# Kernel optimization log

Hardware: AMD Instinct MI355X
Metric: run time of the kernel (lower is better)

The kernel has to match this reference:

```python
import jax, jax.numpy as jnp
import numpy as np

LRELU_GAIN = 2.0 ** 0.5  # util.lrelu_gain (assumed sqrt(2))
EPS = 1e-8


def upsample2_bilinear_ac(x):
    # F.upsample_bilinear == bilinear with align_corners=True, scale 2
    B, C, H, W = x.shape
    def lerp_axis(t, n, axis):
        c = jnp.arange(2 * n, dtype=jnp.float32) * (n - 1) / (2 * n - 1)
        i0 = jnp.floor(c).astype(jnp.int32)
        i1 = jnp.minimum(i0 + 1, n - 1)
        f = c - i0.astype(jnp.float32)
        a = jnp.take(t, i0, axis=axis)
        b = jnp.take(t, i1, axis=axis)
        shape = [1] * t.ndim
        shape[axis] = 2 * n
        f = f.reshape(shape)
        return a * (1.0 - f) + b * f
    x = lerp_axis(x, H, 2)
    x = lerp_axis(x, W, 3)
    return x


def conv1x1(x, weight, bias, gain):
    # Conv2dNormalizedLR with kernel_size=1: he = gain/sqrt(in)
    cin = weight.shape[1]
    he = gain / float(cin) ** 0.5
    y = jnp.einsum('bihw,oi->bohw', x, weight[:, :, 0, 0] * he)
    return y + bias[None, :, None, None]


def mod_conv3x3(x, weight, style, gain):
    # weight: [Cin, Cout, 3, 3]; style: [B, Cin]
    cin, cout, k, _ = weight.shape
    he = gain / float(cin * k * k) ** 0.5
    wmod = style[:, :, None, None, None] * (weight * he)[None]  # [B,Cin,Cout,k,k]
    # demodulation: normalize over (in, kh, kw) per out channel
    d = jax.lax.rsqrt(jnp.sum(wmod * wmod, axis=(1, 3, 4), keepdims=True) + EPS)
    wmod = wmod * d
    # conv_transpose2d(stride=1, pad=1, k=3) == conv2d with transposed+flipped kernel, pad=1
    kern = jnp.flip(jnp.transpose(wmod, (0, 2, 1, 3, 4)), axis=(3, 4))  # [B,Cout,Cin,k,k]
    def one(xb, kb):
        return jax.lax.conv_general_dilated(
            xb[None], kb, (1, 1), ((1, 1), (1, 1)),
            dimension_numbers=('NCHW', 'OIHW', 'NCHW'))[0]
    y = jax.vmap(one)(x, kern)
    return y * gain


def noise_affine(noise, w_s, b_s, w_b, b_b):
    # Baff*: 1x1 conv from 1 channel, gain=1 -> he=1
    ys = noise * w_s[None, :, 0, None, 0, None][:, :, :, 0] if False else noise * w_s[:, 0, 0, 0][None, :, None, None] + b_s[None, :, None, None]
    yb = noise * w_b[:, 0, 0, 0][None, :, None, None] + b_b[None, :, None, None]
    return ys, yb


def block_forward(x, w, noise1, noise2, conv1_w, bias1, conv2_w, bias2,
                  Aaff1_w, Aaff1_b, Aaff2_w, Aaff2_b,
                  Baff1s_w, Baff1s_b, Baff1b_w, Baff1b_b,
                  Baff2s_w, Baff2s_b, Baff2b_w, Baff2b_b,
                  rgb_w, rgb_b):
    x = upsample2_bilinear_ac(x)
    style1 = conv1x1(w, Aaff1_w, Aaff1_b, 1.0)[:, :, 0, 0]  # [B, Cin]
    x = mod_conv3x3(x, conv1_w, style1, LRELU_GAIN)
    ys, yb = noise_affine(noise1, Baff1s_w, Baff1s_b, Baff1b_w, Baff1b_b)
    x = x * ys + yb + bias1
    x = jax.nn.leaky_relu(x, 0.2)
    style2 = conv1x1(w, Aaff2_w, Aaff2_b, 1.0)[:, :, 0, 0]
    x = mod_conv3x3(x, conv2_w, style2, LRELU_GAIN)
    ys, yb = noise_affine(noise2, Baff2s_w, Baff2s_b, Baff2b_w, Baff2b_b)
    x = x * ys + yb + bias2
    x = jax.nn.leaky_relu(x, 0.2)
    rgb = conv1x1(x, rgb_w, rgb_b, 0.03)
    return x, rgb


def setup_inputs() -> dict:
    key = jax.random.key(0)
    ks = jax.random.split(key, 20)
    B, Cin, Cout, Wd, H, W = 8, 512, 512, 512, 32, 32
    inp = {
        'x': jax.random.normal(ks[0], (B, Cin, H, W), jnp.float32),
        'w': jax.random.normal(ks[1], (B, Wd, 1, 1), jnp.float32),
        'noise1': jax.random.normal(ks[2], (B, 1, 2 * H, 2 * W), jnp.float32),
        'noise2': jax.random.normal(ks[3], (B, 1, 2 * H, 2 * W), jnp.float32),
        'conv1_w': jax.random.normal(ks[4], (Cin, Cout, 3, 3), jnp.float32),
        'bias1': jnp.zeros((1, Cout, 1, 1), jnp.float32),
        'conv2_w': jax.random.normal(ks[5], (Cout, Cout, 3, 3), jnp.float32),
        'bias2': jnp.zeros((1, Cout, 1, 1), jnp.float32),
        'Aaff1_w': jax.random.normal(ks[6], (Cin, Wd, 1, 1), jnp.float32),
        'Aaff1_b': jnp.zeros((Cin,), jnp.float32),
        'Aaff2_w': jax.random.normal(ks[7], (Cout, Wd, 1, 1), jnp.float32),
        'Aaff2_b': jnp.zeros((Cout,), jnp.float32),
        'Baff1s_w': jax.random.normal(ks[8], (Cout, 1, 1, 1), jnp.float32) * 0.1,
        'Baff1s_b': jnp.ones((Cout,), jnp.float32),
        'Baff1b_w': jax.random.normal(ks[9], (Cout, 1, 1, 1), jnp.float32) * 0.1,
        'Baff1b_b': jnp.zeros((Cout,), jnp.float32),
        'Baff2s_w': jax.random.normal(ks[10], (Cout, 1, 1, 1), jnp.float32) * 0.1,
        'Baff2s_b': jnp.ones((Cout,), jnp.float32),
        'Baff2b_w': jax.random.normal(ks[11], (Cout, 1, 1, 1), jnp.float32) * 0.1,
        'Baff2b_b': jnp.zeros((Cout,), jnp.float32),
        'rgb_w': jax.random.normal(ks[12], (3, Cout, 1, 1), jnp.float32),
        'rgb_b': jnp.zeros((3,), jnp.float32),
    }
    return inp


def reference(x, w, noise1, noise2, conv1_w, bias1, conv2_w, bias2,
              Aaff1_w, Aaff1_b, Aaff2_w, Aaff2_b,
              Baff1s_w, Baff1s_b, Baff1b_w, Baff1b_b,
              Baff2s_w, Baff2s_b, Baff2b_w, Baff2b_b,
              rgb_w, rgb_b):
    return block_forward(x, w, noise1, noise2, conv1_w, bias1, conv2_w, bias2,
                         Aaff1_w, Aaff1_b, Aaff2_w, Aaff2_b,
                         Baff1s_w, Baff1s_b, Baff1b_w, Baff1b_b,
                         Baff2s_w, Baff2s_b, Baff2b_w, Baff2b_b,
                         rgb_w, rgb_b)
```

## Files before the change

kernel.cpp:

```cpp
#include <hip/hip_runtime.h>
#include <hip/hip_bf16.h>

#define BB 8
#define CC 512
#define HO 64
#define HP 66
#define NPIX (BB*HO*HO)

typedef float f32x4 __attribute__((ext_vector_type(4)));
typedef __bf16 bf16x8 __attribute__((ext_vector_type(8)));
using bf16 = __hip_bfloat16;

__device__ __forceinline__ void gload16(const void* g, void* l) {
    __builtin_amdgcn_global_load_lds((const __attribute__((address_space(1))) void*)g,
                                     (__attribute__((address_space(3))) void*)l, 16, 0, 0);
}

__device__ __forceinline__ float waveRedSum(float v) {
    #pragma unroll
    for (int off = 32; off; off >>= 1) v += __shfl_down(v, off);
    return v;
}

__global__ void init_all(const float* __restrict__ W1, const float* __restrict__ W2,
                         float* __restrict__ S21, float* __restrict__ S22,
                         bf16* __restrict__ kT1, bf16* __restrict__ kT2, float he,
                         bf16* __restrict__ xs1, bf16* __restrict__ xs2,
                         const float* __restrict__ rgbb, float* __restrict__ outrgb) {
    int blk = blockIdx.x, tid = threadIdx.x;
    if (blk < 2048) {
        int which = blk >> 10;
        const float* Wsrc = which ? W2 : W1;
        float* S2ho = which ? S22 : S21;
        bf16* keffT = which ? kT2 : kT1;
        int t = ((blk & 1023) << 8) + tid;
        int i = t & (CC-1), o = t >> 9;
        const float* wp = Wsrc + (i*CC + o)*9;
        float v[9]; float s2 = 0.f;
        #pragma unroll
        for (int k = 0; k < 9; ++k) { v[k] = wp[k] * he; s2 += v[k]*v[k]; }
        S2ho[o*CC + i] = s2;
        #pragma unroll
        for (int tp = 0; tp < 9; ++tp) keffT[(tp*CC + o)*CC + i] = (bf16)v[8 - tp];
    } else if (blk < 3088) {
        int sub = ((blk - 2048) << 2) + (tid >> 6);
        int ln = tid & 63;
        bf16* dst = (sub & 1) ? xs2 : xs1;
        int idx = sub >> 1;
        int b = idx / 260, rm = idx - b*260;
        int p, q;
        if (rm < 66)       { p = 0;        q = rm; }
        else if (rm < 132) { p = 65;       q = rm - 66; }
        else if (rm < 196) { p = rm - 131; q = 0; }
        else               { p = rm - 195; q = 65; }
        f32x4* d4 = (f32x4*)(dst + ((size_t)((b*HP + p)*HP + q)) * CC);
        d4[ln] = f32x4{0.f, 0.f, 0.f, 0.f};
    } else {
        int t2 = ((blk - 3088) << 2) + (tid >> 6);
        int plane = t2 >> 4;
        int c = plane - (plane/3)*3;
        float v = rgbb[c];
        *(f32x4*)(outrgb + (plane << 12) + ((t2 & 15) << 8) + ((tid & 63) << 2)) =
            f32x4{v, v, v, v};
    }
}

__global__ void style_kernel(const float* __restrict__ w,
                             const float* __restrict__ A1, const float* __restrict__ A1b,
                             const float* __restrict__ A2, const float* __restrict__ A2b,
                             float* __restrict__ s1, float* __restrict__ s2) {
    int wid = (blockIdx.x * blockDim.x + threadIdx.x) >> 6;
    int lane = threadIdx.x & 63;
    int set = wid >= BB*CC; int rem = set ? wid - BB*CC : wid;
    int b = rem >> 9, i = rem & (CC-1);
    const float* A = set ? A2 : A1;
    const float* wb = w + b*CC;
    float sum = 0.f;
    for (int d = lane; d < CC; d += 64) sum += wb[d] * A[i*CC + d];
    sum = waveRedSum(sum);
    if (lane == 0) {
        float r = sum * 0.04419417382415922f + (set ? A2b : A1b)[i];
        (set ? s2 : s1)[b*CC + i] = r;
    }
}

__global__ void demod_kernel(const float* __restrict__ s1, const float* __restrict__ S21,
                             const float* __restrict__ s2, const float* __restrict__ S22,
                             float* __restrict__ dg1, float* __restrict__ dg2, float gain) {
    int wid = (blockIdx.x * blockDim.x + threadIdx.x) >> 6;
    int lane = threadIdx.x & 63;
    int set = wid >= BB*CC; int rem = set ? wid - BB*CC : wid;
    int b = rem >> 9, o = rem & (CC-1);
    const float* st = (set ? s2 : s1) + b*CC;
    const float* S2 = (set ? S22 : S21) + o*CC;
    float sum = 0.f;
    for (int i = lane; i < CC; i += 64) { float sv = st[i]; sum += sv*sv*S2[i]; }
    sum = waveRedSum(sum);
    if (lane == 0) (set ? dg2 : dg1)[b*CC + o] = gain * rsqrtf(sum + 1e-8f);
}

__global__ void upsample_mod(const float* __restrict__ x, const float* __restrict__ s1,
                             bf16* __restrict__ xs1) {
    __shared__ float usl[32][CC];
    int blk = blockIdx.x;
    int i = threadIdx.x;
    int b = blk >> 6, p = blk & 63;
    const float scale = 31.0f / 63.0f;
    float chf = p * scale; int h0 = (int)chf; float fh = chf - h0; int h1 = min(h0 + 1, 31);
    const float* xb = x + ((size_t)(b*CC + i) << 10);
    #pragma unroll
    for (int k = 0; k < 8; ++k) {
        f32x4 r0 = *(const f32x4*)(xb + (h0 << 5) + (k << 2));
        f32x4 r1 = *(const f32x4*)(xb + (h1 << 5) + (k << 2));
        #pragma unroll
        for (int e = 0; e < 4; ++e)
            usl[(k << 2) + e][i] = r0[e]*(1.f - fh) + r1[e]*fh;
    }
    float sv = s1[b*CC + i];
    bf16* op = xs1 + ((size_t)((b*HP + p + 1)*HP + 1))*CC + i;
    #pragma unroll
    for (int q = 0; q < 64; ++q) {
        float cwf = q * scale; int w0 = (int)cwf; float fw = cwf - w0;
        int w1 = min(w0 + 1, 31);
        float v = (usl[w0][i]*(1.f - fw) + usl[w1][i]*fw) * sv;
        op[q*CC] = (bf16)v;
    }
}

#define SB  __builtin_amdgcn_sched_barrier(0)
#define BAR __builtin_amdgcn_s_barrier()
#define VMC(n)  asm volatile("s_waitcnt vmcnt(" #n ")" ::: "memory")

#define STAGE_A(d, h, U) do { \
    gload16((U) + aThr + (h)*(HP*1024),                 ldsA + (d)*32768 + (h)*16384); \
    gload16((U) + aThr + (h)*(HP*1024) + 2*(HP*1024),   ldsA + (d)*32768 + (h)*16384 + 8192); \
} while (0)

#define STAGE_B(d, h, U) do { \
    gload16((U) + bThr + (h)*32768,                     ldsB + (d)*32768 + (h)*16384); \
    gload16((U) + bThr + (h)*32768 + 131072,            ldsB + (d)*32768 + (h)*16384 + 8192); \
} while (0)

#define LOAD_A(d, fh) do { \
    _Pragma("unroll") \
    for (int fmq = 0; fmq < 4; ++fmq) { \
        afr[fmq][0] = *(const bf16x8*)(aRd + (d)*32768 + (fh)*16384 + fmq*2048 + swz0); \
        afr[fmq][1] = *(const bf16x8*)(aRd + (d)*32768 + (fh)*16384 + fmq*2048 + swz1); \
    } } while (0)

#define LOAD_B(d, nh) do { \
    _Pragma("unroll") \
    for (int fnq = 0; fnq < 2; ++fnq) { \
        bfr[nh][fnq][0] = *(const bf16x8*)(bRd + (d)*32768 + (nh)*16384 + fnq*2048 + swz0); \
        bfr[nh][fnq][1] = *(const bf16x8*)(bRd + (d)*32768 + (nh)*16384 + fnq*2048 + swz1); \
    } } while (0)

#define QUAD(fh, nh) do { \
    __builtin_amdgcn_s_setprio(1); \
    _Pragma("unroll") \
    for (int kc = 0; kc < 2; ++kc) \
    { _Pragma("unroll") \
      for (int fmq = 0; fmq < 4; ++fmq) \
      { _Pragma("unroll") \
        for (int fnq = 0; fnq < 2; ++fnq) \
            acc[(fh)*4+fmq][(nh)*2+fnq] = __builtin_amdgcn_mfma_f32_16x16x32_bf16( \
                afr[fmq][kc], bfr[nh][fnq][kc], acc[(fh)*4+fmq][(nh)*2+fnq], 0, 0, 0); } } \
    __builtin_amdgcn_s_setprio(0); } while (0)

#define KSTEP(cur, nxt, aN, bN, doStage) do { \
    if (doStage) { \
        STAGE_A(nxt, 0, aN); STAGE_A(nxt, 1, aN); \
        STAGE_B(nxt, 0, bN); STAGE_B(nxt, 1, bN); \
    } \
    LOAD_A(cur, 0); LOAD_B(cur, 0); \
    QUAD(0, 0); \
    LOAD_B(cur, 1); \
    QUAD(0, 1); \
    LOAD_A(cur, 1); \
    QUAD(1, 1); \
    QUAD(1, 0); \
    VMC(0); SB; BAR; SB; \
} while (0)

#define CONV_COMMON \
    __shared__ __attribute__((aligned(16))) bf16 As[32768]; \
    __shared__ __attribute__((aligned(16))) bf16 Bs[32768]; \
    const int tid = threadIdx.x; \
    const int wave = tid >> 6, lane = tid & 63; \
    const int tileId = ((blockIdx.x & 7) << 5) + (blockIdx.x >> 3); \
    const int mtile = tileId >> 1, ntile = tileId & 1; \
    const int m0 = mtile << 8, n0 = ntile << 8; \
    const int b  = m0 >> 12; \
    const int p0 = (m0 & 4095) >> 6; \
    const int wm = wave >> 2, wn = wave & 3; \
    const int l15 = lane & 15; \
    const int srcSwz = (((tid & 7) ^ ((tid >> 3) & 7)) << 4); \
    const int aThr = ((tid >> 3) << 10) + srcSwz; \
    const int bThr = (((tid >> 8) & 1) << 16) + (((tid >> 3) & 31) << 10) + srcSwz; \
    char* const ldsA = (char*)As + tid*16; \
    char* const ldsB = (char*)Bs + tid*16; \
    const char* const aRd = (const char*)As + (((wm << 6) + l15) << 7); \
    const char* const bRd = (const char*)Bs + (((wn << 5) + l15) << 7); \
    const int swz0 = (((lane >> 4)    ) ^ (lane & 7)) << 4; \
    const int swz1 = (((lane >> 4) | 4) ^ (lane & 7)) << 4; \
    f32x4 acc[8][4]; \
    _Pragma("unroll") \
    for (int i_ = 0; i_ < 8; ++i_) \
        _Pragma("unroll") \
        for (int j_ = 0; j_ < 4; ++j_) acc[i_][j_] = f32x4{0.f, 0.f, 0.f, 0.f}; \
    bf16x8 afr[4][2], bfr[2][2][2]; \
    auto abase = [&](int st) -> const char* { \
        int t = st >> 3; int dh = (t*11) >> 5; int dw = t - dh*3; \
        return (const char*)xs + ((size_t)((b*HP + p0 + dh)*HP + dw) << 10) + ((st & 7) << 7); \
    }; \
    auto bbase = [&](int st) -> const char* { \
        int t = st >> 3; \
        return (const char*)keffT + ((size_t)(t*CC + n0) << 10) + ((st & 7) << 7); \
    }; \
    { \
        const char* a0 = abase(0); const char* b0 = bbase(0); \
        STAGE_A(0, 0, a0); STAGE_A(0, 1, a0); \
        STAGE_B(0, 0, b0); STAGE_B(0, 1, b0); \
        VMC(0); SB; BAR; SB; \
    } \
    _Pragma("unroll 1") \
    for (int it = 0; it < 36; ++it) { \
        const bool more = (it < 35); \
        const char* aE = abase(2*it + 1); const char* bE = bbase(2*it + 1); \
        const char* aO = abase(2*it + 2); const char* bO = bbase(2*it + 2); \
        KSTEP(0, 1, aE, bE, true); \
        KSTEP(1, 0, aO, bO, more); \
    }

__global__ __launch_bounds__(512, 2) void conv_gemm1(
    const bf16* __restrict__ xs, const bf16* __restrict__ keffT,
    const float* __restrict__ dg, const float* __restrict__ noise,
    const float* __restrict__ nsw, const float* __restrict__ nsb,
    const float* __restrict__ nbw, const float* __restrict__ nbb,
    const float* __restrict__ biasv, const float* __restrict__ stnext,
    bf16* __restrict__ outb) {
    CONV_COMMON
    const float* dgb = dg + b*CC;
    int nIdx[4]; float pdg[4], pnsw[4], pnsb[4], pnbw[4], pnbb[4], pbias[4], pst[4];
    #pragma unroll
    for (int fn = 0; fn < 4; ++fn) {
        int n = n0 + (wn << 6) + (fn << 4) + l15;
        nIdx[fn] = n;
        pdg[fn] = dgb[n]; pnsw[fn] = nsw[n]; pnsb[fn] = nsb[n];
        pnbw[fn] = nbw[n]; pnbb[fn] = nbb[n]; pbias[fn] = biasv[n];
        pst[fn] = stnext[b*CC + n];
    }
    #pragma unroll
    for (int fm = 0; fm < 8; ++fm) {
        const int mbase = m0 + (wm << 7) + (fm << 4) + ((lane >> 4) << 2);
        const f32x4 nsv = *(const f32x4*)(noise + mbase);
        #pragma unroll
        for (int r = 0; r < 4; ++r) {
            int mloc = mbase + r;
            float ns = nsv[r];
            int prow = (mloc & 4095) >> 6, qcol = mloc & 63;
            #pragma unroll
            for (int fn = 0; fn < 4; ++fn) {
                float v = acc[fm][fn][r] * pdg[fn];
                v = v * (ns*pnsw[fn] + pnsb[fn]) + (ns*pnbw[fn] + pnbb[fn]) + pbias[fn];
                v = fmaxf(v, 0.2f*v);
                outb[(((b*HP) + prow + 1)*HP + (qcol + 1))*CC + nIdx[fn]] =
                    (bf16)(v * pst[fn]);
            }
        }
    }
}

__global__ __launch_bounds__(512, 2) void conv_gemm2(
    const bf16* __restrict__ xs, const bf16* __restrict__ keffT,
    const float* __restrict__ dg, const float* __restrict__ noise,
    const float* __restrict__ nsw, const float* __restrict__ nsb,
    const float* __restrict__ nbw, const float* __restrict__ nbb,
    const float* __restrict__ biasv, float* __restrict__ outf,
    const float* __restrict__ rgbwv, float* __restrict__ outrgb) {
    CONV_COMMON
    const float* dgb = dg + b*CC;
    int nIdx[4]; float pdg[4], pnsw[4], pnsb[4], pnbw[4], pnbb[4], pbias[4];
    float w0[4], w1[4], w2[4];
    const float heR = 0.03f * 0.04419417382415922f;
    #pragma unroll
    for (int fn = 0; fn < 4; ++fn) {
        int n = n0 + (wn << 6) + (fn << 4) + l15;
        nIdx[fn] = n;
        pdg[fn] = dgb[n]; pnsw[fn] = nsw[n]; pnsb[fn] = nsb[n];
        pnbw[fn] = nbw[n]; pnbb[fn] = nbb[n]; pbias[fn] = biasv[n];
        w0[fn] = rgbwv[n] * heR;
        w1[fn] = rgbwv[CC + n] * heR;
        w2[fn] = rgbwv[2*CC + n] * heR;
    }
    #pragma unroll
    for (int fm = 0; fm < 8; ++fm) {
        const int mbase = m0 + (wm << 7) + (fm << 4) + ((lane >> 4) << 2);
        const f32x4 nsv = *(const f32x4*)(noise + mbase);
        f32x4 pc0 = {0.f,0.f,0.f,0.f}, pc1 = {0.f,0.f,0.f,0.f}, pc2 = {0.f,0.f,0.f,0.f};
        #pragma unroll
        for (int fn = 0; fn < 4; ++fn) {
            f32x4 vv;
            #pragma unroll
            for (int r = 0; r < 4; ++r) {
                float ns = nsv[r];
                float v = acc[fm][fn][r] * pdg[fn];
                v = v * (ns*pnsw[fn] + pnsb[fn]) + (ns*pnbw[fn] + pnbb[fn]) + pbias[fn];
                vv[r] = fmaxf(v, 0.2f*v);
            }
            pc0 += vv * w0[fn]; pc1 += vv * w1[fn]; pc2 += vv * w2[fn];
            *(f32x4*)(outf + ((size_t)(b*CC + nIdx[fn]) << 12) + (mbase & 4095)) = vv;
        }
        #pragma unroll
        for (int r = 0; r < 4; ++r) {
            float a0 = pc0[r], a1 = pc1[r], a2 = pc2[r];
            #pragma unroll
            for (int mk = 1; mk < 16; mk <<= 1) {
                a0 += __shfl_xor(a0, mk);
                a1 += __shfl_xor(a1, mk);
                a2 += __shfl_xor(a2, mk);
            }
            if (l15 < 3) {
                float av = (l15 == 0) ? a0 : (l15 == 1) ? a1 : a2;
                int px = (mbase + r) & 4095;
                atomicAdd(outrgb + (b*3 + l15)*4096 + px, av);
            }
        }
    }
}

extern "C" void kernel_launch(void* const* d_in, const int* in_sizes, int n_in,
                              void* d_out, int out_size, void* d_ws, size_t ws_size,
                              hipStream_t stream) {
    const float* x      = (const float*)d_in[0];
    const float* w      = (const float*)d_in[1];
    const float* noise1 = (const float*)d_in[2];
    const float* noise2 = (const float*)d_in[3];
    const float* conv1w = (const float*)d_in[4];
    const float* bias1  = (const float*)d_in[5];
    const float* conv2w = (const float*)d_in[6];
    const float* bias2  = (const float*)d_in[7];
    const float* A1w = (const float*)d_in[8];
    const float* A1b = (const float*)d_in[9];
    const float* A2w = (const float*)d_in[10];
    const float* A2b = (const float*)d_in[11];
    const float* B1sw = (const float*)d_in[12];
    const float* B1sb = (const float*)d_in[13];
    const float* B1bw = (const float*)d_in[14];
    const float* B1bb = (const float*)d_in[15];
    const float* B2sw = (const float*)d_in[16];
    const float* B2sb = (const float*)d_in[17];
    const float* B2bw = (const float*)d_in[18];
    const float* B2bb = (const float*)d_in[19];
    const float* rgbw = (const float*)d_in[20];
    const float* rgbb = (const float*)d_in[21];

    char* ws = (char*)d_ws;
    size_t off = 0;
    auto alloc = [&](size_t bytes) { char* p = ws + off; off += (bytes + 255) & ~(size_t)255; return p; };
    const size_t xsBytes = (size_t)BB*HP*HP*CC*2;
    bf16* xs1 = (bf16*)alloc(xsBytes);
    bf16* xs2 = (bf16*)alloc(xsBytes);
    bf16* kT1 = (bf16*)alloc((size_t)9*CC*CC*2);
    bf16* kT2 = (bf16*)alloc((size_t)9*CC*CC*2);
    float* S21 = (float*)alloc((size_t)CC*CC*4);
    float* S22 = (float*)alloc((size_t)CC*CC*4);
    float* s1  = (float*)alloc(BB*CC*4);
    float* s2  = (float*)alloc(BB*CC*4);
    float* dg1 = (float*)alloc(BB*CC*4);
    float* dg2 = (float*)alloc(BB*CC*4);

    float* outx   = (float*)d_out;
    float* outrgb = outx + (size_t)BB*CC*HO*HO;

    const float gain = 1.41421356237309515f;
    const float he = gain / sqrtf(512.f * 9.f);
    init_all<<<3184, 256, 0, stream>>>(conv1w, conv2w, S21, S22, kT1, kT2, he,
                                       xs1, xs2, rgbb, outrgb);
    style_kernel<<<2*BB*CC/4, 256, 0, stream>>>(w, A1w, A1b, A2w, A2b, s1, s2);
    demod_kernel<<<2*BB*CC/4, 256, 0, stream>>>(s1, S21, s2, S22, dg1, dg2, gain);
    upsample_mod<<<BB*HO, CC, 0, stream>>>(x, s1, xs1);
    conv_gemm1<<<(NPIX/256)*(CC/256), 512, 0, stream>>>(
        xs1, kT1, dg1, noise1, B1sw, B1sb, B1bw, B1bb, bias1, s2, xs2);
    conv_gemm2<<<(NPIX/256)*(CC/256), 512, 0, stream>>>(
        xs2, kT2, dg2, noise2, B2sw, B2sb, B2bw, B2bb, bias2, outx, rgbw, outrgb);
}
```

Baseline: 318.1 us.

## Shrink conv GEMM tiles to 128x128 with 4-wave blocks

The implicit-GEMM conv kernels move from 256x256 tiles with 8 waves to 128x128 tiles with 4 waves, each wave owning a 64x64 sub-tile. The LDS staging, fragment loads and MFMA loop are rebuilt to match, and the grid grows from 256 to 1024 blocks. The goal is to fill all CUs more evenly and improve occupancy, at the cost of halving operand reuse per tile and doubling global/LDS traffic per FLOP.

```diff
diff --git a/kernel.cpp b/kernel.cpp
--- a/kernel.cpp
+++ b/kernel.cpp
@@ -130,85 +130,81 @@
 #define SB  __builtin_amdgcn_sched_barrier(0)
 #define BAR __builtin_amdgcn_s_barrier()
 #define VMC(n)  asm volatile("s_waitcnt vmcnt(" #n ")" ::: "memory")
-
-#define STAGE_A(d, h, U) do { \
-    gload16((U) + aThr + (h)*(HP*1024),                 ldsA + (d)*32768 + (h)*16384); \
-    gload16((U) + aThr + (h)*(HP*1024) + 2*(HP*1024),   ldsA + (d)*32768 + (h)*16384 + 8192); \
+#define HPB (HP*1024)
+
+#define STAGE_A(d, U) do { \
+    gload16((U) + aThr,                   ldsA + (d)*16384); \
+    gload16((U) + aThr + 32768,           ldsA + (d)*16384 + 4096); \
+    gload16((U) + aThr + HPB,             ldsA + (d)*16384 + 8192); \
+    gload16((U) + aThr + HPB + 32768,     ldsA + (d)*16384 + 12288); \
 } while (0)
 
-#define STAGE_B(d, h, U) do { \
-    gload16((U) + bThr + (h)*32768,                     ldsB + (d)*32768 + (h)*16384); \
-    gload16((U) + bThr + (h)*32768 + 131072,            ldsB + (d)*32768 + (h)*16384 + 8192); \
+#define STAGE_B(d, U) do { \
+    gload16((U) + bThr,                   ldsB + (d)*16384); \
+    gload16((U) + bThr + 32768,           ldsB + (d)*16384 + 4096); \
+    gload16((U) + bThr + 65536,           ldsB + (d)*16384 + 8192); \
+    gload16((U) + bThr + 98304,           ldsB + (d)*16384 + 12288); \
 } while (0)
 
-#define LOAD_A(d, fh) do { \
+#define LOAD_A_K(d, kc) do { \
     _Pragma("unroll") \
-    for (int fmq = 0; fmq < 4; ++fmq) { \
-        afr[fmq][0] = *(const bf16x8*)(aRd + (d)*32768 + (fh)*16384 + fmq*2048 + swz0); \
-        afr[fmq][1] = *(const bf16x8*)(aRd + (d)*32768 + (fh)*16384 + fmq*2048 + swz1); \
-    } } while (0)
-
-#define LOAD_B(d, nh) do { \
+    for (int fmq = 0; fmq < 4; ++fmq) \
+        afr[fmq][kc] = *(const bf16x8*)(aRd + (d)*16384 + fmq*2048 + ((kc) ? swz1 : swz0)); \
+    } while (0)
+
+#define LOAD_B_K(d, kc) do { \
     _Pragma("unroll") \
-    for (int fnq = 0; fnq < 2; ++fnq) { \
-        bfr[nh][fnq][0] = *(const bf16x8*)(bRd + (d)*32768 + (nh)*16384 + fnq*2048 + swz0); \
-        bfr[nh][fnq][1] = *(const bf16x8*)(bRd + (d)*32768 + (nh)*16384 + fnq*2048 + swz1); \
-    } } while (0)
-
-#define QUAD(fh, nh) do { \
+    for (int fnq = 0; fnq < 4; ++fnq) \
+        bfr[fnq][kc] = *(const bf16x8*)(bRd + (d)*16384 + fnq*2048 + ((kc) ? swz1 : swz0)); \
+    } while (0)
+
+#define MFMA_K(kc) do { \
     __builtin_amdgcn_s_setprio(1); \
     _Pragma("unroll") \
-    for (int kc = 0; kc < 2; ++kc) \
+    for (int fmq = 0; fmq < 4; ++fmq) \
     { _Pragma("unroll") \
-      for (int fmq = 0; fmq < 4; ++fmq) \
-      { _Pragma("unroll") \
-        for (int fnq = 0; fnq < 2; ++fnq) \
-            acc[(fh)*4+fmq][(nh)*2+fnq] = __builtin_amdgcn_mfma_f32_16x16x32_bf16( \
-                afr[fmq][kc], bfr[nh][fnq][kc], acc[(fh)*4+fmq][(nh)*2+fnq], 0, 0, 0); } } \
+      for (int fnq = 0; fnq < 4; ++fnq) \
+        acc[fmq][fnq] = __builtin_amdgcn_mfma_f32_16x16x32_bf16( \
+            afr[fmq][kc], bfr[fnq][kc], acc[fmq][fnq], 0, 0, 0); } \
     __builtin_amdgcn_s_setprio(0); } while (0)
 
 #define KSTEP(cur, nxt, aN, bN, doStage) do { \
-    if (doStage) { \
-        STAGE_A(nxt, 0, aN); STAGE_A(nxt, 1, aN); \
-        STAGE_B(nxt, 0, bN); STAGE_B(nxt, 1, bN); \
-    } \
-    LOAD_A(cur, 0); LOAD_B(cur, 0); \
-    QUAD(0, 0); \
-    LOAD_B(cur, 1); \
-    QUAD(0, 1); \
-    LOAD_A(cur, 1); \
-    QUAD(1, 1); \
-    QUAD(1, 0); \
+    if (doStage) { STAGE_A(nxt, aN); STAGE_B(nxt, bN); } \
+    LOAD_A_K(cur, 0); LOAD_B_K(cur, 0); \
+    MFMA_K(0); \
+    LOAD_A_K(cur, 1); LOAD_B_K(cur, 1); \
+    MFMA_K(1); \
     VMC(0); SB; BAR; SB; \
 } while (0)
 
 #define CONV_COMMON \
-    __shared__ __attribute__((aligned(16))) bf16 As[32768]; \
-    __shared__ __attribute__((aligned(16))) bf16 Bs[32768]; \
+    __shared__ __attribute__((aligned(16))) bf16 As[16384];   \
+    __shared__ __attribute__((aligned(16))) bf16 Bs[16384];   \
     const int tid = threadIdx.x; \
     const int wave = tid >> 6, lane = tid & 63; \
-    const int tileId = ((blockIdx.x & 7) << 5) + (blockIdx.x >> 3); \
-    const int mtile = tileId >> 1, ntile = tileId & 1; \
-    const int m0 = mtile << 8, n0 = ntile << 8; \
+     \
+    const int tileId = ((blockIdx.x & 7) << 7) + (blockIdx.x >> 3); \
+    const int mtile = tileId >> 2, ntile = tileId & 3; \
+    const int m0 = mtile << 7, n0 = ntile << 7; \
     const int b  = m0 >> 12; \
     const int p0 = (m0 & 4095) >> 6; \
-    const int wm = wave >> 2, wn = wave & 3; \
+    const int wm = wave >> 1, wn = wave & 1; \
     const int l15 = lane & 15; \
-    const int srcSwz = (((tid & 7) ^ ((tid >> 3) & 7)) << 4); \
-    const int aThr = ((tid >> 3) << 10) + srcSwz; \
-    const int bThr = (((tid >> 8) & 1) << 16) + (((tid >> 3) & 31) << 10) + srcSwz; \
+    const int preswz = (((tid & 7) ^ ((tid >> 3) & 7)) << 4); \
+    const int aThr = ((tid >> 3) << 10) + preswz; \
+    const int bThr = ((tid >> 3) << 10) + preswz; \
     char* const ldsA = (char*)As + tid*16; \
     char* const ldsB = (char*)Bs + tid*16; \
     const char* const aRd = (const char*)As + (((wm << 6) + l15) << 7); \
-    const char* const bRd = (const char*)Bs + (((wn << 5) + l15) << 7); \
+    const char* const bRd = (const char*)Bs + (((wn << 6) + l15) << 7); \
     const int swz0 = (((lane >> 4)    ) ^ (lane & 7)) << 4; \
     const int swz1 = (((lane >> 4) | 4) ^ (lane & 7)) << 4; \
-    f32x4 acc[8][4]; \
+    f32x4 acc[4][4]; \
     _Pragma("unroll") \
-    for (int i_ = 0; i_ < 8; ++i_) \
+    for (int i_ = 0; i_ < 4; ++i_) \
         _Pragma("unroll") \
         for (int j_ = 0; j_ < 4; ++j_) acc[i_][j_] = f32x4{0.f, 0.f, 0.f, 0.f}; \
-    bf16x8 afr[4][2], bfr[2][2][2]; \
+    bf16x8 afr[4][2], bfr[4][2]; \
     auto abase = [&](int st) -> const char* { \
         int t = st >> 3; int dh = (t*11) >> 5; int dw = t - dh*3; \
         return (const char*)xs + ((size_t)((b*HP + p0 + dh)*HP + dw) << 10) + ((st & 7) << 7); \
@@ -219,8 +215,7 @@
     }; \
     { \
         const char* a0 = abase(0); const char* b0 = bbase(0); \
-        STAGE_A(0, 0, a0); STAGE_A(0, 1, a0); \
-        STAGE_B(0, 0, b0); STAGE_B(0, 1, b0); \
+        STAGE_A(0, a0); STAGE_B(0, b0); \
         VMC(0); SB; BAR; SB; \
     } \
     _Pragma("unroll 1") \
@@ -232,7 +227,7 @@
         KSTEP(1, 0, aO, bO, more); \
     }
 
-__global__ __launch_bounds__(512, 2) void conv_gemm1(
+__global__ __launch_bounds__(256, 2) void conv_gemm1(
     const bf16* __restrict__ xs, const bf16* __restrict__ keffT,
     const float* __restrict__ dg, const float* __restrict__ noise,
     const float* __restrict__ nsw, const float* __restrict__ nsb,
@@ -251,8 +246,8 @@
         pst[fn] = stnext[b*CC + n];
     }
     #pragma unroll
-    for (int fm = 0; fm < 8; ++fm) {
-        const int mbase = m0 + (wm << 7) + (fm << 4) + ((lane >> 4) << 2);
+    for (int fm = 0; fm < 4; ++fm) {
+        const int mbase = m0 + (wm << 6) + (fm << 4) + ((lane >> 4) << 2);
         const f32x4 nsv = *(const f32x4*)(noise + mbase);
         #pragma unroll
         for (int r = 0; r < 4; ++r) {
@@ -271,7 +266,7 @@
     }
 }
 
-__global__ __launch_bounds__(512, 2) void conv_gemm2(
+__global__ __launch_bounds__(256, 2) void conv_gemm2(
     const bf16* __restrict__ xs, const bf16* __restrict__ keffT,
     const float* __restrict__ dg, const float* __restrict__ noise,
     const float* __restrict__ nsw, const float* __restrict__ nsb,
@@ -294,8 +289,8 @@
         w2[fn] = rgbwv[2*CC + n] * heR;
     }
     #pragma unroll
-    for (int fm = 0; fm < 8; ++fm) {
-        const int mbase = m0 + (wm << 7) + (fm << 4) + ((lane >> 4) << 2);
+    for (int fm = 0; fm < 4; ++fm) {
+        const int mbase = m0 + (wm << 6) + (fm << 4) + ((lane >> 4) << 2);
         const f32x4 nsv = *(const f32x4*)(noise + mbase);
         f32x4 pc0 = {0.f,0.f,0.f,0.f}, pc1 = {0.f,0.f,0.f,0.f}, pc2 = {0.f,0.f,0.f,0.f};
         #pragma unroll
@@ -380,8 +375,8 @@
     style_kernel<<<2*BB*CC/4, 256, 0, stream>>>(w, A1w, A1b, A2w, A2b, s1, s2);
     demod_kernel<<<2*BB*CC/4, 256, 0, stream>>>(s1, S21, s2, S22, dg1, dg2, gain);
     upsample_mod<<<BB*HO, CC, 0, stream>>>(x, s1, xs1);
-    conv_gemm1<<<(NPIX/256)*(CC/256), 512, 0, stream>>>(
+    conv_gemm1<<<(NPIX/128)*(CC/128), 256, 0, stream>>>(
         xs1, kT1, dg1, noise1, B1sw, B1sb, B1bw, B1bb, bias1, s2, xs2);
-    conv_gemm2<<<(NPIX/256)*(CC/256), 512, 0, stream>>>(
+    conv_gemm2<<<(NPIX/128)*(CC/128), 256, 0, stream>>>(
         xs2, kT2, dg2, noise2, B2sw, B2sb, B2bw, B2bb, bias2, outx, rgbw, outrgb);
 }
```

Result: slower. 354.1 us (+11.3%).
